# Optimization experiments

Measured on AMD Instinct MI355X. Metric: run time of the kernel, lower is better.

The kernel has to match this reference:

```python
import jax, jax.numpy as jnp
import numpy as np

E = 256      # embedding_dim
H = 8        # num_heads
D = E // H   # head_dim = 32
F = 1024     # dim_feedforward
EPS = 1e-5


def layer_norm(x, gamma, beta):
    mu = jnp.mean(x, axis=-1, keepdims=True)
    var = jnp.var(x, axis=-1, keepdims=True)
    return (x - mu) * jax.lax.rsqrt(var + EPS) * gamma + beta


def setup_inputs() -> dict:
    key = jax.random.key(0)
    ks = jax.random.split(key, 12)
    s = lambda fan_in: 1.0 / np.sqrt(fan_in)
    src = jax.random.normal(ks[0], (4, 2048, E), dtype=jnp.float32)
    w_in = jax.random.uniform(ks[1], (3 * E, E), minval=-s(E), maxval=s(E), dtype=jnp.float32)
    w_out = jax.random.uniform(ks[2], (E, E), minval=-s(E), maxval=s(E), dtype=jnp.float32)
    w1 = jax.random.uniform(ks[3], (F, E), minval=-s(E), maxval=s(E), dtype=jnp.float32)
    b1 = jax.random.uniform(ks[4], (F,), minval=-s(E), maxval=s(E), dtype=jnp.float32)
    w2 = jax.random.uniform(ks[5], (E, F), minval=-s(F), maxval=s(F), dtype=jnp.float32)
    b2 = jax.random.uniform(ks[6], (E,), minval=-s(F), maxval=s(F), dtype=jnp.float32)
    g1 = jnp.ones((E,), jnp.float32)
    beta1 = jnp.zeros((E,), jnp.float32)
    g2 = jnp.ones((E,), jnp.float32)
    beta2 = jnp.zeros((E,), jnp.float32)
    return {"src": src, "w_in": w_in, "w_out": w_out, "w1": w1, "b1": b1,
            "w2": w2, "b2": b2, "g1": g1, "beta1": beta1, "g2": g2, "beta2": beta2}


def reference(src, w_in, w_out, w1, b1, w2, b2, g1, beta1, g2, beta2):
    B, S, _ = src.shape
    scale = D ** (-0.5)
    # --- pre-norm self-attention block ---
    x = layer_norm(src, g1, beta1)                 # [B,S,E]
    qkv = x @ w_in.T                               # [B,S,3E]
    q, k, v = jnp.split(qkv, 3, axis=-1)
    q = q.reshape(B, S, H, D).transpose(0, 2, 1, 3)  # [B,H,S,D]
    k = k.reshape(B, S, H, D).transpose(0, 2, 1, 3)
    v = v.reshape(B, S, H, D).transpose(0, 2, 1, 3)
    scores = jnp.einsum('bhqd,bhkd->bhqk', q, k) * scale  # [B,H,S,S]
    attn = jax.nn.softmax(scores, axis=-1)
    out = jnp.einsum('bhqk,bhkd->bhqd', attn, v)   # [B,H,S,D]
    out = out.transpose(0, 2, 1, 3).reshape(B, S, E)
    src = src + out @ w_out.T
    # --- pre-norm FFN block ---
    y = layer_norm(src, g2, beta2)
    y = jax.nn.relu(y @ w1.T + b1) @ w2.T + b2
    return src + y
```

## Files before the change

### kernel.cpp

```cpp
#include <hip/hip_runtime.h>
#include <hip/hip_bf16.h>
#include <math.h>

typedef unsigned short u16;
typedef unsigned int   u32;
using bf16x8 = __attribute__((ext_vector_type(8))) short;
using f32x4  = __attribute__((ext_vector_type(4))) float;
using f32x16 = __attribute__((ext_vector_type(16))) float;
using u32v4  = __attribute__((ext_vector_type(4))) u32;

#define TE 256
#define TH 8
#define TS 2048
#define TB 4
#define NTOK 8192
#define QSCALE 0.2550120651552454f
#define EXP2(x) __builtin_amdgcn_exp2f(x)

__device__ __forceinline__ void async16(const u16* g, u16* l) {
    __builtin_amdgcn_global_load_lds(
        (const __attribute__((address_space(1))) u32*)g,
        (__attribute__((address_space(3))) u32*)l, 16, 0, 0);
}
__device__ __forceinline__ u32 pkbf(float a, float b) {
    u32 ua = __float_as_uint(a) + 0x8000u;
    u32 ub = __float_as_uint(b) + 0x8000u;
    return __builtin_amdgcn_perm(ub, ua, 0x07060302u);
}
__device__ __forceinline__ u16 bf1(float a) {
    return (u16)((__float_as_uint(a) + 0x8000u) >> 16);
}

__device__ __forceinline__ void ln_body(const float* __restrict__ in,
        u16* __restrict__ out, const float* __restrict__ gamma,
        const float* __restrict__ beta, int rowblk) {
    int row  = rowblk * 4 + (threadIdx.x >> 6);
    int lane = threadIdx.x & 63;
    float4 v = ((const float4*)(in + (size_t)row * TE))[lane];
    float s  = v.x + v.y + v.z + v.w;
    float s2 = v.x*v.x + v.y*v.y + v.z*v.z + v.w*v.w;
    #pragma unroll
    for (int off = 32; off > 0; off >>= 1) {
        s  += __shfl_down(s,  off, 64);
        s2 += __shfl_down(s2, off, 64);
    }
    s  = __shfl(s,  0, 64);
    s2 = __shfl(s2, 0, 64);
    float mu = s * (1.f / TE);
    float rs = rsqrtf(s2 * (1.f / TE) - mu * mu + 1e-5f);
    float4 g = ((const float4*)gamma)[lane];
    float4 b = ((const float4*)beta )[lane];
    u32 lo = pkbf((v.x - mu) * rs * g.x + b.x, (v.y - mu) * rs * g.y + b.y);
    u32 hi = pkbf((v.z - mu) * rs * g.z + b.z, (v.w - mu) * rs * g.w + b.w);
    ((uint2*)(out + (size_t)row * TE))[lane] = make_uint2(lo, hi);
}

__global__ __launch_bounds__(256) void ln_bf(const float* __restrict__ in,
        u16* __restrict__ out, const float* __restrict__ gamma,
        const float* __restrict__ beta) {
    ln_body(in, out, gamma, beta, blockIdx.x);
}

__global__ __launch_bounds__(256) void prep(const float* __restrict__ s0, u16* d0,
        const float* __restrict__ s1, u16* d1, const float* __restrict__ s2, u16* d2,
        const float* __restrict__ s3, u16* d3, const float* __restrict__ src,
        u16* __restrict__ xb, const float* __restrict__ g1,
        const float* __restrict__ be1) {
    if (blockIdx.x < 768) {
        int i = (blockIdx.x * 256 + threadIdx.x) * 4;
        const float* s; u16* d;
        if      (i < 196608) { s = s0; d = d0; }
        else if (i < 262144) { s = s1; d = d1; i -= 196608; }
        else if (i < 524288) { s = s2; d = d2; i -= 262144; }
        else                 { s = s3; d = d3; i -= 524288; }
        float4 v = *(const float4*)(s + i);
        *(uint2*)(d + i) = make_uint2(pkbf(v.x, v.y), pkbf(v.z, v.w));
    } else {
        ln_body(src, xb, g1, be1, blockIdx.x - 768);
    }
}

template<int K, int BM, int EPI>
__global__ __launch_bounds__(256) void mgemm(const u16* __restrict__ A,
        const u16* __restrict__ W, const float* __restrict__ bias,
        const float* __restrict__ R, float* __restrict__ Cf,
        u16* __restrict__ Cb, int M) {
    constexpr int BN = BM;
    constexpr int NS = K / 32;
    __shared__ u16 Al[2][BM * 32];
    __shared__ u16 Wl[2][BN * 32];
    const int tid = threadIdx.x, w = tid >> 6, l = tid & 63;
    const int n0 = blockIdx.y * BM;
    const int m0 = blockIdx.x * BN;
    constexpr int NT = (BM == 128) ? 4 : 2;
    constexpr int NF = (BM == 128) ? 4 : 2;
    const int tw = (w & 1) * NT * 16;
    const int fw = (w >> 1) * NF * 16;
    const int fr = l & 15, fq = l >> 4;
    const int sr = l >> 2, sc = (l & 3) * 8;
    f32x4 acc[NT][NF];
    #pragma unroll
    for (int t = 0; t < NT; t++)
        #pragma unroll
        for (int f = 0; f < NF; f++)
            #pragma unroll
            for (int r = 0; r < 4; r++) acc[t][f][r] = 0.f;

    auto stage = [&](int s, int buf) {
        const int kc = s * 32;
        if constexpr (BM == 128) {
            #pragma unroll
            for (int c = 0; c < 2; c++) {
                const int rr = (w * 2 + c) * 16 + sr;
                async16(A + (size_t)(n0 + rr) * K + kc + sc, &Al[buf][(w * 2 + c) * 512]);
                async16(W + (size_t)(m0 + rr) * K + kc + sc, &Wl[buf][(w * 2 + c) * 512]);
            }
        } else {
            const int rr = w * 16 + sr;
            async16(A + (size_t)(n0 + rr) * K + kc + sc, &Al[buf][w * 512]);
            async16(W + (size_t)(m0 + rr) * K + kc + sc, &Wl[buf][w * 512]);
        }
    };

    stage(0, 0);
    __syncthreads();
    #pragma unroll 2
    for (int s = 0; s < NS; ++s) {
        const int buf = s & 1;
        if (s + 1 < NS) stage(s + 1, buf ^ 1);
        bf16x8 af[NT], wf[NF];
        #pragma unroll
        for (int t = 0; t < NT; t++)
            af[t] = *(const bf16x8*)&Al[buf][(tw + t * 16 + fr) * 32 + fq * 8];
        #pragma unroll
        for (int f = 0; f < NF; f++)
            wf[f] = *(const bf16x8*)&Wl[buf][(fw + f * 16 + fr) * 32 + fq * 8];
        #pragma unroll
        for (int t = 0; t < NT; t++)
            #pragma unroll
            for (int f = 0; f < NF; f++)
                acc[t][f] = __builtin_amdgcn_mfma_f32_16x16x32_bf16(
                    wf[f], af[t], acc[t][f], 0, 0, 0);
        __syncthreads();
    }
    #pragma unroll
    for (int t = 0; t < NT; t++) {
        const int tok = n0 + tw + t * 16 + fr;
        #pragma unroll
        for (int f = 0; f < NF; f++) {
            const int fb = m0 + fw + f * 16 + fq * 4;
            f32x4 v = acc[t][f];
            if (EPI == 0) {
                if (fb < 256) {
                    *(uint2*)(Cb + (size_t)tok * 256 + fb) = make_uint2(
                        pkbf(v[0]*QSCALE, v[1]*QSCALE), pkbf(v[2]*QSCALE, v[3]*QSCALE));
                } else if (fb < 512) {
                    const int hh = (fb - 256) >> 5, dd = (fb - 256) & 31;
                    const int bh = (tok >> 11) * 8 + hh;
                    const int kv = tok & 2047, tile = kv >> 5, lq = kv & 31;
                    const int fg = dd >> 4, hg = (dd >> 3) & 1, j = dd & 7;
                    u16* kp = (u16*)bias +
                        (((((size_t)bh * 64 + tile) * 2 + fg) * 2 + hg) * 32 + lq) * 8 + j;
                    *(uint2*)kp = make_uint2(pkbf(v[0], v[1]), pkbf(v[2], v[3]));
                } else {
                    const int hh = (fb - 512) >> 5, dd = (fb - 512) & 31;
                    const int bh = (tok >> 11) * 8 + hh;
                    const int kv = tok & 2047, tile = kv >> 5, kvr = kv & 31;
                    const int fg = kvr >> 4, hg = (kvr >> 3) & 1, j = kvr & 7;
                    u16* vp = (u16*)R +
                        ((((size_t)bh * 64 + tile) * 2 + fg) * 2 + hg) * 256 +
                        (size_t)dd * 8 + j;
                    vp[0]  = bf1(v[0]);
                    vp[8]  = bf1(v[1]);
                    vp[16] = bf1(v[2]);
                    vp[24] = bf1(v[3]);
                }
            } else if (EPI == 1) {
                float4 r4 = *(const float4*)(R + (size_t)tok * M + fb);
                *(float4*)(Cf + (size_t)tok * M + fb) =
                    make_float4(v[0]+r4.x, v[1]+r4.y, v[2]+r4.z, v[3]+r4.w);
            } else if (EPI == 2) {
                float4 b4 = *(const float4*)(bias + fb);
                *(uint2*)(Cb + (size_t)tok * M + fb) = make_uint2(
                    pkbf(fmaxf(v[0]+b4.x, 0.f), fmaxf(v[1]+b4.y, 0.f)),
                    pkbf(fmaxf(v[2]+b4.z, 0.f), fmaxf(v[3]+b4.w, 0.f)));
            } else {
                float4 b4 = *(const float4*)(bias + fb);
                float4 r4 = *(const float4*)(R + (size_t)tok * M + fb);
                *(float4*)(Cf + (size_t)tok * M + fb) = make_float4(
                    v[0]+b4.x+r4.x, v[1]+b4.y+r4.y, v[2]+b4.z+r4.z, v[3]+b4.w+r4.w);
            }
        }
    }
}

__global__ __launch_bounds__(256, 4) void attn_k(const u16* __restrict__ qb,
        const u16* __restrict__ kfb, const u16* __restrict__ vfb,
        u16* __restrict__ attn) {
    const int id = blockIdx.x;
    const int bh   = (id & 7) * 4 + (id >> 8);
    const int tile = (id >> 3) & 31;
    const int b = bh >> 3, h = bh & 7;
    const int tid = threadIdx.x, w = tid >> 6, l = tid & 63;
    const int qw = w & 1, kw = w >> 1;
    const int lq = l & 31, hi = l >> 5;
    const size_t btok = (size_t)b * TS;
    const int q0 = tile * 64 + qw * 32;

    __shared__ float mrg[2304];

    const u16* qrow = qb + (btok + q0 + lq) * 256 + h * 32 + hi * 8;
    bf16x8 qf0 = *(const bf16x8*)qrow;
    bf16x8 qf1 = *(const bf16x8*)(qrow + 16);

    f32x16 zf, o;
    #pragma unroll
    for (int r = 0; r < 16; r++) { zf[r] = 0.f; o[r] = 0.f; }
    float ps = 0.f;

    const u16* kp = kfb + ((size_t)bh * 64 + kw * 32) * 1024 + l * 8;
    const u16* vp = vfb + ((size_t)bh * 64 + kw * 32) * 1024 + l * 8;
    bf16x8 k0 = *(const bf16x8*)kp;
    bf16x8 k1 = *(const bf16x8*)(kp + 512);
    bf16x8 v0 = *(const bf16x8*)vp;
    bf16x8 v1 = *(const bf16x8*)(vp + 512);

    #pragma unroll 2
    for (int it = 0; it < 32; ++it) {
        kp += 1024; vp += 1024;
        bf16x8 nk0 = *(const bf16x8*)kp;
        bf16x8 nk1 = *(const bf16x8*)(kp + 512);
        bf16x8 nv0 = *(const bf16x8*)vp;
        bf16x8 nv1 = *(const bf16x8*)(vp + 512);
        f32x16 p = __builtin_amdgcn_mfma_f32_32x32x16_bf16(k0, qf0, zf, 0, 0, 0);
        p = __builtin_amdgcn_mfma_f32_32x32x16_bf16(k1, qf1, p, 0, 0, 0);
        float e[16];
        #pragma unroll
        for (int r = 0; r < 16; r++) e[r] = EXP2(p[r]);
        ps += ((e[0]+e[1]) + (e[2]+e[3])) + ((e[4]+e[5]) + (e[6]+e[7]))
            + ((e[8]+e[9]) + (e[10]+e[11])) + ((e[12]+e[13]) + (e[14]+e[15]));
        u32 a[8];
        #pragma unroll
        for (int j = 0; j < 8; j++)
            asm("v_cvt_pk_bf16_f32 %0, %1, %2"
                : "=v"(a[j]) : "v"(e[2*j]), "v"(e[2*j+1]));
        asm("v_permlane32_swap_b32 %0, %1" : "+v"(a[0]), "+v"(a[2]));
        asm("v_permlane32_swap_b32 %0, %1" : "+v"(a[1]), "+v"(a[3]));
        asm("v_permlane32_swap_b32 %0, %1" : "+v"(a[4]), "+v"(a[6]));
        asm("v_permlane32_swap_b32 %0, %1" : "+v"(a[5]), "+v"(a[7]));
        u32v4 t0 = {a[0], a[1], a[2], a[3]};
        u32v4 t1 = {a[4], a[5], a[6], a[7]};
        bf16x8 pf0 = __builtin_bit_cast(bf16x8, t0);
        bf16x8 pf1 = __builtin_bit_cast(bf16x8, t1);
        o = __builtin_amdgcn_mfma_f32_32x32x16_bf16(v0, pf0, o, 0, 0, 0);
        o = __builtin_amdgcn_mfma_f32_32x32x16_bf16(v1, pf1, o, 0, 0, 0);
        k0 = nk0; k1 = nk1; v0 = nv0; v1 = nv1;
    }
    ps += __shfl_xor(ps, 32, 64);

    if (kw == 1) {
        float* d = mrg + (qw * 64 + l) * 18;
        #pragma unroll
        for (int r = 0; r < 16; r++) d[r] = o[r];
        d[16] = ps;
    }
    __syncthreads();
    if (kw == 0) {
        const float* d = mrg + (qw * 64 + l) * 18;
        #pragma unroll
        for (int r = 0; r < 16; r++) o[r] += d[r];
        ps += d[16];
        float inv = 1.f / ps;
        int tok = (int)btok + q0 + lq;
        u16* orow = attn + (size_t)tok * 256 + h * 32 + hi * 4;
        #pragma unroll
        for (int g = 0; g < 4; g++)
            *(uint2*)(orow + g * 8) = make_uint2(
                pkbf(o[4*g]*inv, o[4*g+1]*inv), pkbf(o[4*g+2]*inv, o[4*g+3]*inv));
    }
}

extern "C" void kernel_launch(void* const* d_in, const int* in_sizes, int n_in,
                              void* d_out, int out_size, void* d_ws, size_t ws_size,
                              hipStream_t stream) {
    const float* src  = (const float*)d_in[0];
    const float* w_in = (const float*)d_in[1];
    const float* w_out= (const float*)d_in[2];
    const float* w1   = (const float*)d_in[3];
    const float* b1   = (const float*)d_in[4];
    const float* w2   = (const float*)d_in[5];
    const float* b2   = (const float*)d_in[6];
    const float* g1   = (const float*)d_in[7];
    const float* be1  = (const float*)d_in[8];
    const float* g2   = (const float*)d_in[9];
    const float* be2  = (const float*)d_in[10];
    float* out = (float*)d_out;

    u16* xb    = (u16*)d_ws;
    u16* qb    = xb + (size_t)NTOK * 256;
    u16* kfbuf = qb + (size_t)NTOK * 256;
    u16* vfbuf = kfbuf + (size_t)32 * 64 * 1024;
    u16* attnb = xb;
    u16* h1b   = (u16*)d_ws;
    u16* x2b   = (u16*)((char*)d_ws + (size_t)NTOK * 1024 * 2);
    u16* wib   = x2b + (size_t)NTOK * 256;
    u16* wob   = wib + 768 * 256;
    u16* w1b   = wob + 256 * 256;
    u16* w2b   = w1b + 1024 * 256;

    prep<<<768 + NTOK / 4, 256, 0, stream>>>(
        w_in, wib, w_out, wob, w1, w1b, w2, w2b, src, xb, g1, be1);
    mgemm<256, 128, 0><<<dim3(6, 64), 256, 0, stream>>>(
        xb, wib, (const float*)kfbuf, (const float*)vfbuf, nullptr, qb, 768);
    attn_k<<<dim3(1024), 256, 0, stream>>>(qb, kfbuf, vfbuf, attnb);
    mgemm<256, 64, 1><<<dim3(4, 128), 256, 0, stream>>>(
        attnb, wob, nullptr, src, out, nullptr, 256);
    ln_bf<<<NTOK / 4, 256, 0, stream>>>(out, x2b, g2, be2);
    mgemm<256, 128, 2><<<dim3(8, 64), 256, 0, stream>>>(
        x2b, w1b, b1, nullptr, nullptr, h1b, 1024);
    mgemm<1024, 64, 3><<<dim3(4, 128), 256, 0, stream>>>(
        h1b, w2b, b2, out, out, nullptr, 256);
}
```

Measured before the change: 166.4 us.

## Fuse out-projection GEMM with residual and LayerNorm, remap GEMM blocks per XCD

Replaces the out-projection GEMM, the separate residual epilogue and the standalone LayerNorm kernel with one kernel, g4ln. Each 512-thread block computes a full 32-token row slab across all 256 output columns, writes the residual sum, and normalizes it from shared memory into the bf16 input for the FFN. The remaining GEMMs switch to a 1D grid whose block index is remapped so consecutive blocks on the same XCD share row tiles, aiming at better L2 reuse. The cost is one fewer launch and one fewer full-tensor round trip, in exchange for only 256 blocks with a small 32-token tile in the fused kernel, which may reduce parallelism.

```diff
diff --git a/kernel.cpp b/kernel.cpp
--- a/kernel.cpp
+++ b/kernel.cpp
@@ -53,12 +53,6 @@
     u32 lo = pkbf((v.x - mu) * rs * g.x + b.x, (v.y - mu) * rs * g.y + b.y);
     u32 hi = pkbf((v.z - mu) * rs * g.z + b.z, (v.w - mu) * rs * g.w + b.w);
     ((uint2*)(out + (size_t)row * TE))[lane] = make_uint2(lo, hi);
-}
-
-__global__ __launch_bounds__(256) void ln_bf(const float* __restrict__ in,
-        u16* __restrict__ out, const float* __restrict__ gamma,
-        const float* __restrict__ beta) {
-    ln_body(in, out, gamma, beta, blockIdx.x);
 }
 
 __global__ __launch_bounds__(256) void prep(const float* __restrict__ s0, u16* d0,
@@ -80,7 +74,7 @@
     }
 }
 
-template<int K, int BM, int EPI>
+template<int K, int BM, int EPI, int NYL>
 __global__ __launch_bounds__(256) void mgemm(const u16* __restrict__ A,
         const u16* __restrict__ W, const float* __restrict__ bias,
         const float* __restrict__ R, float* __restrict__ Cf,
@@ -89,9 +83,11 @@
     constexpr int NS = K / 32;
     __shared__ u16 Al[2][BM * 32];
     __shared__ u16 Wl[2][BN * 32];
+    const int id = blockIdx.x;
+    const int xcd = id & 7, sq = id >> 3;
+    const int n0 = (xcd * (1 << NYL) + (sq & ((1 << NYL) - 1))) * BM;
+    const int m0 = (sq >> NYL) * BN;
     const int tid = threadIdx.x, w = tid >> 6, l = tid & 63;
-    const int n0 = blockIdx.y * BM;
-    const int m0 = blockIdx.x * BN;
     constexpr int NT = (BM == 128) ? 4 : 2;
     constexpr int NF = (BM == 128) ? 4 : 2;
     const int tw = (w & 1) * NT * 16;
@@ -175,10 +171,6 @@
                     vp[16] = bf1(v[2]);
                     vp[24] = bf1(v[3]);
                 }
-            } else if (EPI == 1) {
-                float4 r4 = *(const float4*)(R + (size_t)tok * M + fb);
-                *(float4*)(Cf + (size_t)tok * M + fb) =
-                    make_float4(v[0]+r4.x, v[1]+r4.y, v[2]+r4.z, v[3]+r4.w);
             } else if (EPI == 2) {
                 float4 b4 = *(const float4*)(bias + fb);
                 *(uint2*)(Cb + (size_t)tok * M + fb) = make_uint2(
@@ -191,6 +183,84 @@
                     v[0]+b4.x+r4.x, v[1]+b4.y+r4.y, v[2]+b4.z+r4.z, v[3]+b4.w+r4.w);
             }
         }
+    }
+}
+
+__global__ __launch_bounds__(512) void g4ln(const u16* __restrict__ A,
+        const u16* __restrict__ W, const float* __restrict__ src,
+        float* __restrict__ out, u16* __restrict__ x2b,
+        const float* __restrict__ g2, const float* __restrict__ be2) {
+    __shared__ __align__(16) char smem[36864];
+    u16* Al = (u16*)smem;
+    u16* Wl = (u16*)(smem + 4096);
+    const int tid = threadIdx.x, w = tid >> 6, l = tid & 63;
+    const int tg = w & 1, fg = w >> 1;
+    const int fr = l & 15, fq = l >> 4;
+    const int sr = l >> 2, sc = (l & 3) * 8;
+    const int n0 = blockIdx.x * 32;
+    f32x4 acc[4];
+    #pragma unroll
+    for (int f = 0; f < 4; f++)
+        #pragma unroll
+        for (int r = 0; r < 4; r++) acc[f][r] = 0.f;
+
+    auto stage = [&](int st, int buf) {
+        const int kc = st * 32;
+        const int rr = w * 16 + sr;
+        async16(W + (size_t)rr * 256 + kc + sc, &Wl[buf * 8192 + w * 512]);
+        async16(W + (size_t)(rr + 128) * 256 + kc + sc, &Wl[buf * 8192 + 4096 + w * 512]);
+        if (w < 2) async16(A + (size_t)(n0 + rr) * 256 + kc + sc, &Al[buf * 1024 + w * 512]);
+    };
+
+    stage(0, 0);
+    __syncthreads();
+    #pragma unroll 2
+    for (int st = 0; st < 8; ++st) {
+        const int buf = st & 1;
+        if (st + 1 < 8) stage(st + 1, buf ^ 1);
+        bf16x8 af = *(const bf16x8*)&Al[buf * 1024 + (tg * 16 + fr) * 32 + fq * 8];
+        bf16x8 wf[4];
+        #pragma unroll
+        for (int f = 0; f < 4; f++)
+            wf[f] = *(const bf16x8*)&Wl[buf * 8192 + (fg * 64 + f * 16 + fr) * 32 + fq * 8];
+        #pragma unroll
+        for (int f = 0; f < 4; f++)
+            acc[f] = __builtin_amdgcn_mfma_f32_16x16x32_bf16(wf[f], af, acc[f], 0, 0, 0);
+        __syncthreads();
+    }
+    float* T = (float*)smem;
+    const int tokl = tg * 16 + fr;
+    const int tok  = n0 + tokl;
+    #pragma unroll
+    for (int f = 0; f < 4; ++f) {
+        const int fb = fg * 64 + f * 16 + fq * 4;
+        float4 s4 = *(const float4*)(src + (size_t)tok * 256 + fb);
+        f32x4 v = acc[f];
+        float4 o4 = make_float4(v[0]+s4.x, v[1]+s4.y, v[2]+s4.z, v[3]+s4.w);
+        *(float4*)(out + (size_t)tok * 256 + fb) = o4;
+        *(float4*)&T[tokl * 260 + fb] = o4;
+    }
+    __syncthreads();
+    float4 gg = ((const float4*)g2)[l];
+    float4 bb = ((const float4*)be2)[l];
+    #pragma unroll
+    for (int rr = 0; rr < 4; ++rr) {
+        const int r = w * 4 + rr;
+        float4 x = *(const float4*)&T[r * 260 + l * 4];
+        float s  = x.x + x.y + x.z + x.w;
+        float s2 = x.x*x.x + x.y*x.y + x.z*x.z + x.w*x.w;
+        #pragma unroll
+        for (int off = 32; off > 0; off >>= 1) {
+            s  += __shfl_down(s,  off, 64);
+            s2 += __shfl_down(s2, off, 64);
+        }
+        s  = __shfl(s,  0, 64);
+        s2 = __shfl(s2, 0, 64);
+        float mu = s * (1.f / 256.f);
+        float rs = rsqrtf(s2 * (1.f / 256.f) - mu * mu + 1e-5f);
+        u32 lo = pkbf((x.x - mu) * rs * gg.x + bb.x, (x.y - mu) * rs * gg.y + bb.y);
+        u32 hi = pkbf((x.z - mu) * rs * gg.z + bb.z, (x.w - mu) * rs * gg.w + bb.w);
+        *(uint2*)(x2b + (size_t)(n0 + r) * 256 + l * 4) = make_uint2(lo, hi);
     }
 }
 
@@ -310,14 +380,12 @@
 
     prep<<<768 + NTOK / 4, 256, 0, stream>>>(
         w_in, wib, w_out, wob, w1, w1b, w2, w2b, src, xb, g1, be1);
-    mgemm<256, 128, 0><<<dim3(6, 64), 256, 0, stream>>>(
+    mgemm<256, 128, 0, 3><<<384, 256, 0, stream>>>(
         xb, wib, (const float*)kfbuf, (const float*)vfbuf, nullptr, qb, 768);
     attn_k<<<dim3(1024), 256, 0, stream>>>(qb, kfbuf, vfbuf, attnb);
-    mgemm<256, 64, 1><<<dim3(4, 128), 256, 0, stream>>>(
-        attnb, wob, nullptr, src, out, nullptr, 256);
-    ln_bf<<<NTOK / 4, 256, 0, stream>>>(out, x2b, g2, be2);
-    mgemm<256, 128, 2><<<dim3(8, 64), 256, 0, stream>>>(
+    g4ln<<<256, 512, 0, stream>>>(attnb, wob, src, out, x2b, g2, be2);
+    mgemm<256, 128, 2, 3><<<512, 256, 0, stream>>>(
         x2b, w1b, b1, nullptr, nullptr, h1b, 1024);
-    mgemm<1024, 64, 3><<<dim3(4, 128), 256, 0, stream>>>(
+    mgemm<1024, 64, 3, 4><<<512, 256, 0, stream>>>(
         h1b, w2b, b2, out, out, nullptr, 256);
 }
```

Measured after the change: 169.1 us. No clear change (+1.6%).

## Triple-buffer GEMM LDS staging with explicit vmcnt waits and one barrier per step

Applied to the files above, without the earlier changes.

The GEMM k-loop moves from double to triple buffering of its async global-to-LDS loads. It prefetches two stages ahead, waits with explicit s_waitcnt vmcnt counts, and uses a single barrier per iteration instead of two __syncthreads. The aim is to hide global load latency behind the MFMA work and cut synchronisation stalls, at the cost of more shared memory per block, which may lower occupancy. The prep kernel is also split back into a separate weight-conversion kernel and a layernorm kernel, which adds one launch.

```diff
diff --git a/kernel.cpp b/kernel.cpp
--- a/kernel.cpp
+++ b/kernel.cpp
@@ -30,11 +30,16 @@
 __device__ __forceinline__ u16 bf1(float a) {
     return (u16)((__float_as_uint(a) + 0x8000u) >> 16);
 }
-
-__device__ __forceinline__ void ln_body(const float* __restrict__ in,
+template<int N> __device__ __forceinline__ void waitv() {
+    if constexpr (N == 0)      asm volatile("s_waitcnt vmcnt(0)" ::: "memory");
+    else if constexpr (N == 2) asm volatile("s_waitcnt vmcnt(2)" ::: "memory");
+    else                       asm volatile("s_waitcnt vmcnt(4)" ::: "memory");
+}
+
+__global__ __launch_bounds__(256) void ln_bf(const float* __restrict__ in,
         u16* __restrict__ out, const float* __restrict__ gamma,
-        const float* __restrict__ beta, int rowblk) {
-    int row  = rowblk * 4 + (threadIdx.x >> 6);
+        const float* __restrict__ beta) {
+    int row  = blockIdx.x * 4 + (threadIdx.x >> 6);
     int lane = threadIdx.x & 63;
     float4 v = ((const float4*)(in + (size_t)row * TE))[lane];
     float s  = v.x + v.y + v.z + v.w;
@@ -55,29 +60,17 @@
     ((uint2*)(out + (size_t)row * TE))[lane] = make_uint2(lo, hi);
 }
 
-__global__ __launch_bounds__(256) void ln_bf(const float* __restrict__ in,
-        u16* __restrict__ out, const float* __restrict__ gamma,
-        const float* __restrict__ beta) {
-    ln_body(in, out, gamma, beta, blockIdx.x);
-}
-
-__global__ __launch_bounds__(256) void prep(const float* __restrict__ s0, u16* d0,
+__global__ __launch_bounds__(256) void convw(const float* __restrict__ s0, u16* d0,
         const float* __restrict__ s1, u16* d1, const float* __restrict__ s2, u16* d2,
-        const float* __restrict__ s3, u16* d3, const float* __restrict__ src,
-        u16* __restrict__ xb, const float* __restrict__ g1,
-        const float* __restrict__ be1) {
-    if (blockIdx.x < 768) {
-        int i = (blockIdx.x * 256 + threadIdx.x) * 4;
-        const float* s; u16* d;
-        if      (i < 196608) { s = s0; d = d0; }
-        else if (i < 262144) { s = s1; d = d1; i -= 196608; }
-        else if (i < 524288) { s = s2; d = d2; i -= 262144; }
-        else                 { s = s3; d = d3; i -= 524288; }
-        float4 v = *(const float4*)(s + i);
-        *(uint2*)(d + i) = make_uint2(pkbf(v.x, v.y), pkbf(v.z, v.w));
-    } else {
-        ln_body(src, xb, g1, be1, blockIdx.x - 768);
-    }
+        const float* __restrict__ s3, u16* d3) {
+    int i = (blockIdx.x * 256 + threadIdx.x) * 4;
+    const float* s; u16* d;
+    if      (i < 196608) { s = s0; d = d0; }
+    else if (i < 262144) { s = s1; d = d1; i -= 196608; }
+    else if (i < 524288) { s = s2; d = d2; i -= 262144; }
+    else                 { s = s3; d = d3; i -= 524288; }
+    float4 v = *(const float4*)(s + i);
+    *(uint2*)(d + i) = make_uint2(pkbf(v.x, v.y), pkbf(v.z, v.w));
 }
 
 template<int K, int BM, int EPI>
@@ -87,8 +80,9 @@
         u16* __restrict__ Cb, int M) {
     constexpr int BN = BM;
     constexpr int NS = K / 32;
-    __shared__ u16 Al[2][BM * 32];
-    __shared__ u16 Wl[2][BN * 32];
+    constexpr int L  = (BM == 128) ? 4 : 2;
+    __shared__ u16 Al[3][BM * 32];
+    __shared__ u16 Wl[3][BN * 32];
     const int tid = threadIdx.x, w = tid >> 6, l = tid & 63;
     const int n0 = blockIdx.y * BM;
     const int m0 = blockIdx.x * BN;
@@ -123,11 +117,15 @@
     };
 
     stage(0, 0);
-    __syncthreads();
-    #pragma unroll 2
+    stage(1, 1);
+    #pragma unroll
     for (int s = 0; s < NS; ++s) {
-        const int buf = s & 1;
-        if (s + 1 < NS) stage(s + 1, buf ^ 1);
+        const int buf = s % 3;
+        if (s < NS - 1) waitv<L>();
+        else            waitv<0>();
+        __builtin_amdgcn_s_barrier();
+        __builtin_amdgcn_sched_barrier(0);
+        if (s + 2 < NS) stage(s + 2, (s + 2) % 3);
         bf16x8 af[NT], wf[NF];
         #pragma unroll
         for (int t = 0; t < NT; t++)
@@ -141,7 +139,6 @@
             for (int f = 0; f < NF; f++)
                 acc[t][f] = __builtin_amdgcn_mfma_f32_16x16x32_bf16(
                     wf[f], af[t], acc[t][f], 0, 0, 0);
-        __syncthreads();
     }
     #pragma unroll
     for (int t = 0; t < NT; t++) {
@@ -308,8 +305,8 @@
     u16* w1b   = wob + 256 * 256;
     u16* w2b   = w1b + 1024 * 256;
 
-    prep<<<768 + NTOK / 4, 256, 0, stream>>>(
-        w_in, wib, w_out, wob, w1, w1b, w2, w2b, src, xb, g1, be1);
+    convw<<<768, 256, 0, stream>>>(w_in, wib, w_out, wob, w1, w1b, w2, w2b);
+    ln_bf<<<NTOK / 4, 256, 0, stream>>>(src, xb, g1, be1);
     mgemm<256, 128, 0><<<dim3(6, 64), 256, 0, stream>>>(
         xb, wib, (const float*)kfbuf, (const float*)vfbuf, nullptr, qb, 768);
     attn_k<<<dim3(1024), 256, 0, stream>>>(qb, kfbuf, vfbuf, attnb);
```

New measurement: 164.0 us. About the same (-1.5%).
